# Performance work log

Hardware: AMD Instinct MI355X
Metric: run time of the kernel (lower is better)

The kernel has to match this reference:

```python
import jax, jax.numpy as jnp
import numpy as np

DIM, HEADS, DHEAD = 256, 8, 64
HID = HEADS * DHEAD


def _elu1(x):
    # F.elu(x) + 1 == exp(x) for x<0, x+1 for x>=0
    return jnp.where(x > 0, x + 1.0, jnp.exp(x))


def setup_inputs() -> dict:
    key = jax.random.key(0)
    ks = jax.random.split(key, 6)
    B, H, W = 8, 64, 64
    x = jax.random.normal(ks[0], (B, DIM, H, W), dtype=jnp.float32)
    contact_map = jax.random.uniform(ks[1], (B, 1, H, W), dtype=jnp.float32)
    s_qkv = 1.0 / np.sqrt(DIM)
    Wqkv = jax.random.normal(ks[2], (3 * HID, DIM), dtype=jnp.float32) * s_qkv
    s_out = 1.0 / np.sqrt(HID)
    Wout = jax.random.normal(ks[3], (DIM, HID), dtype=jnp.float32) * s_out
    bout = jax.random.normal(ks[4], (DIM,), dtype=jnp.float32) * 0.01
    contact_scale = jnp.float32(0.1)
    return {"x": x, "contact_map": contact_map, "Wqkv": Wqkv,
            "Wout": Wout, "bout": bout, "contact_scale": contact_scale}


def reference(x, contact_map, Wqkv, Wout, bout, contact_scale):
    b, c, h, w = x.shape
    n = h * w
    xf = x.reshape(b, c, n)                                  # b c n
    qkv = jnp.einsum('oc,bcn->bon', Wqkv, xf)                # b (3*H*D) n
    qkv = qkv.reshape(b, 3, HEADS, DHEAD, n)                 # qkv-major channel order
    q = _elu1(qkv[:, 0])                                     # b h d n
    k = _elu1(qkv[:, 1])
    v = qkv[:, 2]
    cm = contact_map.reshape(b, 1, 1, n)                     # b 1 1 n
    k = k * (1.0 + contact_scale * cm)
    kv = jnp.einsum('bhdn,bhen->bhde', k, v)                 # b h d e
    ksum = k.sum(axis=-1)                                    # b h d
    z = 1.0 / (jnp.einsum('bhdn,bhd->bhn', q, ksum) + 1e-6)  # b h n
    out = jnp.einsum('bhde,bhdn->bhne', kv, q) * z[..., None]  # b h n e
    out = out.transpose(0, 1, 3, 2).reshape(b, HID, n)       # b (h d) n
    y = jnp.einsum('oc,bcn->bon', Wout, out) + bout[None, :, None]
    return y.reshape(b, -1, h, w)
```

## Files before the change

kernel.cpp:

```cpp
#include <hip/hip_runtime.h>
#include <stdint.h>


#define NPIX 4096
#define HIDC 512
#define DIMC 256
#define BATCH 8

typedef __attribute__((ext_vector_type(8))) short bf16x8;
typedef __attribute__((ext_vector_type(4))) float f32x4;
typedef __attribute__((ext_vector_type(16))) float f32x16;

__device__ __forceinline__ float bf2f(unsigned short h) {
    unsigned int u = ((unsigned int)h) << 16; float f;
    __builtin_memcpy(&f, &u, 4); return f;
}
__device__ __forceinline__ unsigned short f2bf(float f) {
    unsigned int u; __builtin_memcpy(&u, &f, 4);
    u += 0x7fffu + ((u >> 16) & 1u);
    return (unsigned short)(u >> 16);
}
__device__ __forceinline__ float elu1(float x) {
    return x > 0.f ? x + 1.f : __expf(x);
}
__device__ __forceinline__ void gl16(const unsigned short* g, unsigned short* l) {
    __builtin_amdgcn_global_load_lds(
        (__attribute__((address_space(1))) const void*)g,
        (__attribute__((address_space(3))) void*)l, 16, 0, 0);
}

__global__ __launch_bounds__(256) void k_convW(
    const float* __restrict__ Wqkv, const float* __restrict__ Wout,
    unsigned short* __restrict__ Wb, unsigned short* __restrict__ Wob)
{
    int i4 = (blockIdx.x * 256 + threadIdx.x) * 4;
    const int NW1 = 1536 * 256;
    float4 v; unsigned short* dst;
    if (i4 < NW1) { v = *(const float4*)&Wqkv[i4]; dst = Wb + i4; }
    else { int j = i4 - NW1; v = *(const float4*)&Wout[j]; dst = Wob + j; }
    ushort4 o; o.x = f2bf(v.x); o.y = f2bf(v.y); o.z = f2bf(v.z); o.w = f2bf(v.w);
    *(ushort4*)dst = o;
}

__global__ __launch_bounds__(256) void k_tx(
    const float* __restrict__ x, unsigned short* __restrict__ xT)
{
    __shared__ float tile[32][33];
    const int n0 = blockIdx.x * 32, c0 = blockIdx.y * 32, b = blockIdx.z;
    const int t = threadIdx.x;
    const int r = t >> 3, c4 = (t & 7) * 4;
    float4 v = *(const float4*)&x[((size_t)b * DIMC + c0 + r) * NPIX + n0 + c4];
    tile[r][c4 + 0] = v.x; tile[r][c4 + 1] = v.y;
    tile[r][c4 + 2] = v.z; tile[r][c4 + 3] = v.w;
    __syncthreads();
    ushort4 o;
    unsigned short* op = (unsigned short*)&o;
#pragma unroll
    for (int i = 0; i < 4; i++) op[i] = f2bf(tile[c4 + i][r]);
    *(ushort4*)&xT[((size_t)b * NPIX + n0 + r) * DIMC + c0 + c4] = o;
}


#define COMPUTE_TILE(SWAP, A0, A1)                                             \
    {                                                                          \
        const unsigned short* Wl = &Ws[cur][0];                                \
        _Pragma("unroll")                                                      \
        for (int ks = 0; ks < 16; ks++) {                                      \
            bf16x8 wf = *(const bf16x8*)&Wl[(wn * 32 + l31) * DIMC +           \
                                (((ks * 2 + lhi) ^ (l31 & 7)) * 8)];           \
            if (SWAP) {                                                        \
                A0 = __builtin_amdgcn_mfma_f32_32x32x16_bf16(wf, af[0][ks], A0, 0, 0, 0); \
                A1 = __builtin_amdgcn_mfma_f32_32x32x16_bf16(wf, af[1][ks], A1, 0, 0, 0); \
            } else {                                                           \
                A0 = __builtin_amdgcn_mfma_f32_32x32x16_bf16(af[0][ks], wf, A0, 0, 0, 0); \
                A1 = __builtin_amdgcn_mfma_f32_32x32x16_bf16(af[1][ks], wf, A1, 0, 0, 0); \
            }                                                                  \
        }                                                                      \
    }

__global__ __launch_bounds__(256, 1) void k_fused(
    const unsigned short* __restrict__ xT,
    const unsigned short* __restrict__ Wb,
    const float* __restrict__ cmp,
    const float* __restrict__ csp,
    unsigned short* __restrict__ qT,
    float* __restrict__ kvp,
    float* __restrict__ ksump)
{
    const int b  = blockIdx.y;
    const int m0 = blockIdx.x * 128;
    const int t  = threadIdx.x;
    const int wave = t >> 6, lane = t & 63;
    const int wm = wave >> 1, wn = wave & 1;
    const int l31 = lane & 31, lhi = lane >> 5;

    __shared__ unsigned short Ws[2][64 * DIMC];
    __shared__ unsigned short kS[64 * 128];
    __shared__ unsigned short vS[64 * 128];

    const float cs = *csp;

    auto stageW = [&](int wr, int buf) {
#pragma unroll
        for (int i = 0; i < 8; i++) {
            const int rowl = wave * 16 + i * 2 + (lane >> 5);
            const int ck = (lane & 31) ^ (rowl & 7);
            gl16(&Wb[(size_t)(wr + rowl) * DIMC + ck * 8],
                 &Ws[buf][(wave * 16 + i * 2) * DIMC]);
        }
    };

    stageW(0, 0);

    bf16x8 af[2][16];
    {
        const unsigned short* Ab = xT + ((size_t)b * NPIX + m0 + wm * 64) * DIMC;
#pragma unroll
        for (int pt = 0; pt < 2; pt++)
#pragma unroll
            for (int ks = 0; ks < 16; ks++)
                af[pt][ks] = *(const bf16x8*)&Ab[(size_t)(pt * 32 + l31) * DIMC
                                                 + ks * 16 + lhi * 8];
    }

    const float gv0 = 1.f + cs * cmp[(size_t)b * NPIX + m0 + wm * 64 + l31];
    const float gv1 = 1.f + cs * cmp[(size_t)b * NPIX + m0 + wm * 64 + 32 + l31];

    __syncthreads();
    int cur = 0;

    for (int nt = 0; nt < 8; nt++) {
        stageW(nt < 7 ? (nt + 1) * 64 : 512, cur ^ 1);
        f32x16 acc0, acc1;
#pragma unroll
        for (int r = 0; r < 16; r++) { acc0[r] = 0.f; acc1[r] = 0.f; }
        COMPUTE_TILE(0, acc0, acc1)
        const int chq = nt * 64 + wn * 32 + l31;
        unsigned short* qg = qT + ((size_t)b * NPIX + m0 + wm * 64) * HIDC + chq;
#pragma unroll
        for (int r = 0; r < 16; r++) {
            const int rp = (r & 3) + 8 * (r >> 2) + 4 * lhi;
            qg[(size_t)rp * HIDC]        = f2bf(elu1(acc0[r]));
            qg[(size_t)(32 + rp) * HIDC] = f2bf(elu1(acc1[r]));
        }
        __syncthreads();
        cur ^= 1;
    }

    for (int h = 0; h < 8; h++) {
        stageW(1024 + h * 64, cur ^ 1);
        f32x16 acc0, acc1;
#pragma unroll
        for (int r = 0; r < 16; r++) { acc0[r] = 0.f; acc1[r] = 0.f; }
        COMPUTE_TILE(1, acc0, acc1)
#pragma unroll
        for (int r = 0; r < 16; r++) {
            const int ch = wn * 32 + (r & 3) + 8 * (r >> 2) + 4 * lhi;
            const int sw = (ch & 7) << 3;
            const int p0 = wm * 64 + l31;
            kS[ch * 128 + (p0 ^ sw)]        = f2bf(elu1(acc0[r]) * gv0);
            kS[ch * 128 + ((p0 + 32) ^ sw)] = f2bf(elu1(acc1[r]) * gv1);
        }
        __syncthreads();
        {
            const int ch = t & 63, cb = (t >> 6) * 4;
            float s = 0.f;
#pragma unroll
            for (int j = 0; j < 4; j++) {
                const bf16x8 kr = *(const bf16x8*)&kS[ch * 128 + (((cb + j) ^ (ch & 7)) * 8)];
#pragma unroll
                for (int u = 0; u < 8; u++) s += bf2f(((const unsigned short*)&kr)[u]);
            }
            atomicAdd(&ksump[(size_t)(b * 8 + h) * 64 + ch], s);
        }
        cur ^= 1;

        if (h < 7) stageW(512 + (h + 1) * 64, cur ^ 1);
#pragma unroll
        for (int r = 0; r < 16; r++) { acc0[r] = 0.f; acc1[r] = 0.f; }
        COMPUTE_TILE(1, acc0, acc1)
#pragma unroll
        for (int r = 0; r < 16; r++) {
            const int ch = wn * 32 + (r & 3) + 8 * (r >> 2) + 4 * lhi;
            const int sw = (ch & 7) << 3;
            const int p0 = wm * 64 + l31;
            vS[ch * 128 + (p0 ^ sw)]        = f2bf(acc0[r]);
            vS[ch * 128 + ((p0 + 32) ^ sw)] = f2bf(acc1[r]);
        }
        __syncthreads();

        f32x16 kvacc;
#pragma unroll
        for (int r = 0; r < 16; r++) kvacc[r] = 0.f;
#pragma unroll
        for (int pk = 0; pk < 8; pk++) {
            const int co = (((pk * 2 + lhi) ^ (l31 & 7)) * 8);
            const bf16x8 kf = *(const bf16x8*)&kS[(wm * 32 + l31) * 128 + co];
            const bf16x8 vf = *(const bf16x8*)&vS[(wn * 32 + l31) * 128 + co];
            kvacc = __builtin_amdgcn_mfma_f32_32x32x16_bf16(kf, vf, kvacc, 0, 0, 0);
        }
        __syncthreads();
        float* kvb = kvp + (size_t)(b * 8 + h) * 4096;
#pragma unroll
        for (int r = 0; r < 16; r++) {
            const int d = wm * 32 + (r & 3) + 8 * (r >> 2) + 4 * lhi;
            atomicAdd(&kvb[d * 64 + wn * 32 + l31], kvacc[r]);
        }
        cur ^= 1;
    }
}

#define LS3 72
__global__ __launch_bounds__(256) void k_out(
    const unsigned short* __restrict__ qT,
    const float* __restrict__ kv, const float* __restrict__ ksum,
    unsigned short* __restrict__ outT)
{
    const int bh = blockIdx.y, p0 = blockIdx.x * 128;
    const int b = bh >> 3, h = bh & 7;
    const int t = threadIdx.x, wave = t >> 6, lane = t & 63;
    const int l31 = lane & 31, lhi = lane >> 5;

    __shared__ unsigned short Aq[128 * LS3];
    __shared__ unsigned short Bv[96 * LS3];

    const unsigned short* qg = qT + ((size_t)b * NPIX + p0) * HIDC + h * 64;
#pragma unroll
    for (int i = 0; i < 4; i++) {
        int idx = t + i * 256;
        int row = idx >> 3, c8 = (idx & 7) * 8;
        *(uint4*)&Aq[row * LS3 + c8] = *(const uint4*)&qg[(size_t)row * HIDC + c8];
    }
    const float* kvg = kv + (size_t)bh * 4096;
#pragma unroll
    for (int i = 0; i < 16; i++) {
        int idx = t + i * 256;
        int d = idx >> 6, e = idx & 63;
        Bv[e * LS3 + d] = f2bf(kvg[idx]);
    }
    if (t < 64) {
        float ksv = ksum[bh * 64 + t];
        unsigned short hi = f2bf(ksv);
        Bv[64 * LS3 + t] = hi;
        Bv[65 * LS3 + t] = f2bf(ksv - bf2f(hi));
    }
    for (int i = t; i < 30 * 64; i += 256)
        Bv[(66 + (i >> 6)) * LS3 + (i & 63)] = 0;
    __syncthreads();

    f32x16 acc[3];
#pragma unroll
    for (int j = 0; j < 3; j++)
#pragma unroll
        for (int r = 0; r < 16; r++) acc[j][r] = 0.f;

#pragma unroll
    for (int ksub = 0; ksub < 4; ksub++) {
        const int koff = ksub * 16 + lhi * 8;
        bf16x8 af = *(const bf16x8*)&Aq[(wave * 32 + l31) * LS3 + koff];
#pragma unroll
        for (int nf = 0; nf < 3; nf++) {
            bf16x8 bfg = *(const bf16x8*)&Bv[(nf * 32 + l31) * LS3 + koff];
            acc[nf] = __builtin_amdgcn_mfma_f32_32x32x16_bf16(af, bfg, acc[nf], 0, 0, 0);
        }
    }

    unsigned short* og = outT + ((size_t)b * NPIX + p0 + wave * 32) * HIDC + h * 64;
#pragma unroll
    for (int r = 0; r < 16; r++) {
        float hi = __shfl(acc[2][r], lane & 32);
        float lo = __shfl(acc[2][r], (lane & 32) | 1);
        float z = 1.f / (hi + lo + 1e-6f);
        int prow = (r & 3) + 8 * (r >> 2) + 4 * lhi;
#pragma unroll
        for (int nf = 0; nf < 2; nf++)
            og[(size_t)prow * HIDC + nf * 32 + l31] = f2bf(acc[nf][r] * z);
    }
}

__global__ __launch_bounds__(256) void k_y(
    const unsigned short* __restrict__ outT,
    const unsigned short* __restrict__ Wob,
    const float* __restrict__ bout,
    float* __restrict__ y)
{
    const int b  = blockIdx.z;
    const int m0 = blockIdx.x * 128;
    const int n0 = blockIdx.y * 128;
    const int t = threadIdx.x;
    const int wave = t >> 6, lane = t & 63;
    const int wm = wave >> 1, wn = wave & 1;
    const int lrow = lane & 15, quad = lane >> 4;

    __shared__ unsigned short As[128 * 64];
    __shared__ unsigned short Bs[128 * 64];

    const unsigned short* Ag = outT + ((size_t)b * NPIX + m0) * HIDC;
    const unsigned short* Bg = Wob + (size_t)n0 * HIDC;

    f32x4 acc[4][4];
#pragma unroll
    for (int i = 0; i < 4; i++)
#pragma unroll
        for (int j = 0; j < 4; j++) acc[i][j] = (f32x4){0.f, 0.f, 0.f, 0.f};

    const int r8  = lane >> 3;
    const int jg8 = (((lane & 7) ^ r8) & 7) * 8;
    const int xswA = (lrow & 7);

    for (int k0 = 0; k0 < HIDC; k0 += 64) {
#pragma unroll
        for (int i = 0; i < 4; i++) {
            const int rowg = wave * 32 + i * 8;
            gl16(&Ag[(size_t)(rowg + r8) * HIDC + k0 + jg8], &As[rowg * 64]);
            gl16(&Bg[(size_t)(rowg + r8) * HIDC + k0 + jg8], &Bs[rowg * 64]);
        }
        __syncthreads();
#pragma unroll
        for (int ksb = 0; ksb < 2; ksb++) {
            bf16x8 af[4], bfr[4];
#pragma unroll
            for (int mt = 0; mt < 4; mt++) {
                const int row = wm * 64 + mt * 16 + lrow;
                af[mt] = *(const bf16x8*)&As[row * 64 + (((ksb * 4 + quad) ^ xswA)) * 8];
            }
#pragma unroll
            for (int nt = 0; nt < 4; nt++) {
                const int row = wn * 64 + nt * 16 + lrow;
                bfr[nt] = *(const bf16x8*)&Bs[row * 64 + (((ksb * 4 + quad) ^ xswA)) * 8];
            }
#pragma unroll
            for (int mt = 0; mt < 4; mt++)
#pragma unroll
                for (int nt = 0; nt < 4; nt++)
                    acc[mt][nt] = __builtin_amdgcn_mfma_f32_16x16x32_bf16(
                        af[mt], bfr[nt], acc[mt][nt], 0, 0, 0);
        }
        __syncthreads();
    }

#pragma unroll
    for (int mt = 0; mt < 4; mt++) {
        const int pixel0 = m0 + wm * 64 + mt * 16 + quad * 4;
#pragma unroll
        for (int nt = 0; nt < 4; nt++) {
            const int o = n0 + wn * 64 + nt * 16 + lrow;
            const float bias = bout[o];
            f32x4 a = acc[mt][nt];
            float4 st; st.x = a[0] + bias; st.y = a[1] + bias;
            st.z = a[2] + bias; st.w = a[3] + bias;
            *(float4*)&y[((size_t)b * DIMC + o) * NPIX + pixel0] = st;
        }
    }
}

extern "C" void kernel_launch(void* const* d_in, const int* in_sizes, int n_in,
                              void* d_out, int out_size, void* d_ws, size_t ws_size,
                              hipStream_t stream) {
    (void)in_sizes; (void)n_in; (void)out_size; (void)ws_size;
    const float* x    = (const float*)d_in[0];
    const float* cm   = (const float*)d_in[1];
    const float* Wqkv = (const float*)d_in[2];
    const float* Wout = (const float*)d_in[3];
    const float* bout = (const float*)d_in[4];
    const float* csp  = (const float*)d_in[5];
    float* y = (float*)d_out;

    const size_t qn = (size_t)BATCH * HIDC * NPIX;
    char* ws = (char*)d_ws;
    unsigned short* qT   = (unsigned short*)ws;                 ws += qn * 2;
    unsigned short* outT = (unsigned short*)ws;                 ws += qn * 2;
    unsigned short* xT   = outT;
    float* kvp   = (float*)ws;                                  ws += (size_t)64 * 64 * 64 * 4;
    float* ksump = (float*)ws;                                  ws += (size_t)64 * 64 * 4;
    unsigned short* Wb  = (unsigned short*)ws;                  ws += (size_t)1536 * 256 * 2;
    unsigned short* Wob = (unsigned short*)ws;

    hipMemsetAsync(kvp, 0, ((size_t)64 * 64 * 64 + 64 * 64) * sizeof(float), stream);
    k_convW<<<512, 256, 0, stream>>>(Wqkv, Wout, Wb, Wob);
    k_tx   <<<dim3(128, 8, 8), 256, 0, stream>>>(x, xT);
    k_fused<<<dim3(32, 8),     256, 0, stream>>>(xT, Wb, cm, csp, qT, kvp, ksump);
    k_out  <<<dim3(32, 64),    256, 0, stream>>>(qT, kvp, ksump, outT);
    k_y    <<<dim3(32, 2, 8),  256, 0, stream>>>(outT, Wob, bout, y);
}
```

Baseline: 198.7 us.

## Halve fused QKV pixel tile, split K staging, raise occupancy to two blocks

The fused QKV/kv kernel now processes 64 pixels per block instead of 128, launching twice as many blocks (512 vs 256) with launch bounds allowing two blocks per CU. Weight tiles are staged in K-halves of 128 columns, which halves shared memory and register footprint (one accumulator and 16 A fragments per wave). The kv MFMA for head h is deferred into the next iteration to overlap with weight staging. The cost is more kv/ksum atomics (twice as many blocks contribute), more barriers per tile, and twice as much total weight traffic from L2.

New measurement: 235.8 us. +18.6%, slower.

```diff
diff --git a/kernel.cpp b/kernel.cpp
--- a/kernel.cpp
+++ b/kernel.cpp
@@ -61,24 +61,18 @@
 }
 
 
-#define COMPUTE_TILE(SWAP, A0, A1)                                             \
-    {                                                                          \
-        const unsigned short* Wl = &Ws[cur][0];                                \
-        _Pragma("unroll")                                                      \
-        for (int ks = 0; ks < 16; ks++) {                                      \
-            bf16x8 wf = *(const bf16x8*)&Wl[(wn * 32 + l31) * DIMC +           \
-                                (((ks * 2 + lhi) ^ (l31 & 7)) * 8)];           \
-            if (SWAP) {                                                        \
-                A0 = __builtin_amdgcn_mfma_f32_32x32x16_bf16(wf, af[0][ks], A0, 0, 0, 0); \
-                A1 = __builtin_amdgcn_mfma_f32_32x32x16_bf16(wf, af[1][ks], A1, 0, 0, 0); \
-            } else {                                                           \
-                A0 = __builtin_amdgcn_mfma_f32_32x32x16_bf16(af[0][ks], wf, A0, 0, 0, 0); \
-                A1 = __builtin_amdgcn_mfma_f32_32x32x16_bf16(af[1][ks], wf, A1, 0, 0, 0); \
-            }                                                                  \
-        }                                                                      \
-    }
-
-__global__ __launch_bounds__(256, 1) void k_fused(
+#define CHALF(ACC, KH, BUF, SWAP)                                              \
+    _Pragma("unroll")                                                          \
+    for (int ks = 0; ks < 8; ks++) {                                           \
+        bf16x8 wf = *(const bf16x8*)&Ws[BUF][(wn * 32 + l31) * 128 +           \
+                            (((ks * 2 + lhi) ^ (l31 & 7)) * 8)];               \
+        if (SWAP)                                                              \
+            ACC = __builtin_amdgcn_mfma_f32_32x32x16_bf16(wf, af[(KH) * 8 + ks], ACC, 0, 0, 0); \
+        else                                                                   \
+            ACC = __builtin_amdgcn_mfma_f32_32x32x16_bf16(af[(KH) * 8 + ks], wf, ACC, 0, 0, 0); \
+    }
+
+__global__ __launch_bounds__(256, 2) void k_fused(
     const unsigned short* __restrict__ xT,
     const unsigned short* __restrict__ Wb,
     const float* __restrict__ cmp,
@@ -88,125 +82,141 @@
     float* __restrict__ ksump)
 {
     const int b  = blockIdx.y;
-    const int m0 = blockIdx.x * 128;
+    const int m0 = blockIdx.x * 64;
     const int t  = threadIdx.x;
     const int wave = t >> 6, lane = t & 63;
     const int wm = wave >> 1, wn = wave & 1;
     const int l31 = lane & 31, lhi = lane >> 5;
 
-    __shared__ unsigned short Ws[2][64 * DIMC];
-    __shared__ unsigned short kS[64 * 128];
-    __shared__ unsigned short vS[64 * 128];
+    __shared__ unsigned short Ws[2][64 * 128];
+    __shared__ unsigned short kS[64 * 64];
+    __shared__ unsigned short vS[64 * 64];
 
     const float cs = *csp;
 
-    auto stageW = [&](int wr, int buf) {
-#pragma unroll
-        for (int i = 0; i < 8; i++) {
-            const int rowl = wave * 16 + i * 2 + (lane >> 5);
-            const int ck = (lane & 31) ^ (rowl & 7);
-            gl16(&Wb[(size_t)(wr + rowl) * DIMC + ck * 8],
-                 &Ws[buf][(wave * 16 + i * 2) * DIMC]);
+    auto stageW = [&](int R, int kh, int buf) {
+#pragma unroll
+        for (int i = 0; i < 4; i++) {
+            const int rowbase = wave * 16 + i * 4;
+            const int row = rowbase + (lane >> 4);
+            gl16(&Wb[(size_t)(R + row) * DIMC + kh * 128 +
+                     (((lane & 15) ^ (row & 7)) * 8)],
+                 &Ws[buf][rowbase * 128]);
         }
     };
 
-    stageW(0, 0);
-
-    bf16x8 af[2][16];
+    stageW(0, 0, 0);
+
+    bf16x8 af[16];
     {
-        const unsigned short* Ab = xT + ((size_t)b * NPIX + m0 + wm * 64) * DIMC;
-#pragma unroll
-        for (int pt = 0; pt < 2; pt++)
-#pragma unroll
-            for (int ks = 0; ks < 16; ks++)
-                af[pt][ks] = *(const bf16x8*)&Ab[(size_t)(pt * 32 + l31) * DIMC
-                                                 + ks * 16 + lhi * 8];
-    }
-
-    const float gv0 = 1.f + cs * cmp[(size_t)b * NPIX + m0 + wm * 64 + l31];
-    const float gv1 = 1.f + cs * cmp[(size_t)b * NPIX + m0 + wm * 64 + 32 + l31];
-
-    __syncthreads();
-    int cur = 0;
+        const unsigned short* Ab = xT + ((size_t)b * NPIX + m0 + wm * 32 + l31) * DIMC;
+#pragma unroll
+        for (int ks = 0; ks < 16; ks++)
+            af[ks] = *(const bf16x8*)&Ab[ks * 16 + lhi * 8];
+    }
+    const float gv = 1.f + cs * cmp[(size_t)b * NPIX + m0 + wm * 32 + l31];
 
     for (int nt = 0; nt < 8; nt++) {
-        stageW(nt < 7 ? (nt + 1) * 64 : 512, cur ^ 1);
-        f32x16 acc0, acc1;
-#pragma unroll
-        for (int r = 0; r < 16; r++) { acc0[r] = 0.f; acc1[r] = 0.f; }
-        COMPUTE_TILE(0, acc0, acc1)
-        const int chq = nt * 64 + wn * 32 + l31;
-        unsigned short* qg = qT + ((size_t)b * NPIX + m0 + wm * 64) * HIDC + chq;
+        __syncthreads();
+        stageW(nt * 64, 1, 1);
+        f32x16 acc;
+#pragma unroll
+        for (int r = 0; r < 16; r++) acc[r] = 0.f;
+        CHALF(acc, 0, 0, 0)
+        __syncthreads();
+        stageW(nt < 7 ? (nt + 1) * 64 : 512, 0, 0);
+        CHALF(acc, 1, 1, 0)
+        unsigned short* qg = qT + ((size_t)b * NPIX + m0 + wm * 32) * HIDC
+                           + nt * 64 + wn * 32 + l31;
 #pragma unroll
         for (int r = 0; r < 16; r++) {
             const int rp = (r & 3) + 8 * (r >> 2) + 4 * lhi;
-            qg[(size_t)rp * HIDC]        = f2bf(elu1(acc0[r]));
-            qg[(size_t)(32 + rp) * HIDC] = f2bf(elu1(acc1[r]));
-        }
-        __syncthreads();
-        cur ^= 1;
+            qg[(size_t)rp * HIDC] = f2bf(elu1(acc[r]));
+        }
     }
 
     for (int h = 0; h < 8; h++) {
-        stageW(1024 + h * 64, cur ^ 1);
-        f32x16 acc0, acc1;
-#pragma unroll
-        for (int r = 0; r < 16; r++) { acc0[r] = 0.f; acc1[r] = 0.f; }
-        COMPUTE_TILE(1, acc0, acc1)
+        __syncthreads();
+        stageW(512 + h * 64, 1, 1);
+        if (h > 0) {
+            f32x16 kvacc;
+#pragma unroll
+            for (int r = 0; r < 16; r++) kvacc[r] = 0.f;
+#pragma unroll
+            for (int pk = 0; pk < 4; pk++) {
+                const int co = ((pk * 2 + lhi) ^ (l31 & 7)) * 8;
+                bf16x8 kf = *(const bf16x8*)&kS[(wm * 32 + l31) * 64 + co];
+                bf16x8 vf = *(const bf16x8*)&vS[(wn * 32 + l31) * 64 + co];
+                kvacc = __builtin_amdgcn_mfma_f32_32x32x16_bf16(kf, vf, kvacc, 0, 0, 0);
+            }
+            float* kvb = kvp + (size_t)(b * 8 + (h - 1)) * 4096;
+#pragma unroll
+            for (int r = 0; r < 16; r++) {
+                const int d = wm * 32 + (r & 3) + 8 * (r >> 2) + 4 * lhi;
+                atomicAdd(&kvb[d * 64 + wn * 32 + l31], kvacc[r]);
+            }
+        }
+        f32x16 acc;
+#pragma unroll
+        for (int r = 0; r < 16; r++) acc[r] = 0.f;
+        CHALF(acc, 0, 0, 1)
+        __syncthreads();
+        stageW(1024 + h * 64, 0, 0);
+        CHALF(acc, 1, 1, 1)
 #pragma unroll
         for (int r = 0; r < 16; r++) {
             const int ch = wn * 32 + (r & 3) + 8 * (r >> 2) + 4 * lhi;
-            const int sw = (ch & 7) << 3;
-            const int p0 = wm * 64 + l31;
-            kS[ch * 128 + (p0 ^ sw)]        = f2bf(elu1(acc0[r]) * gv0);
-            kS[ch * 128 + ((p0 + 32) ^ sw)] = f2bf(elu1(acc1[r]) * gv1);
-        }
-        __syncthreads();
+            const int pixl = wm * 32 + l31;
+            kS[ch * 64 + (pixl ^ ((ch & 7) << 3))] = f2bf(elu1(acc[r]) * gv);
+        }
+
+        __syncthreads();
+        stageW(1024 + h * 64, 1, 1);
         {
-            const int ch = t & 63, cb = (t >> 6) * 4;
+            const int ch = t & 63, part = t >> 6;
             float s = 0.f;
 #pragma unroll
-            for (int j = 0; j < 4; j++) {
-                const bf16x8 kr = *(const bf16x8*)&kS[ch * 128 + (((cb + j) ^ (ch & 7)) * 8)];
+            for (int j2 = 0; j2 < 2; j2++) {
+                const int j = part * 2 + j2;
+                const bf16x8 kr = *(const bf16x8*)&kS[ch * 64 + ((j ^ (ch & 7)) * 8)];
 #pragma unroll
                 for (int u = 0; u < 8; u++) s += bf2f(((const unsigned short*)&kr)[u]);
             }
             atomicAdd(&ksump[(size_t)(b * 8 + h) * 64 + ch], s);
         }
-        cur ^= 1;
-
-        if (h < 7) stageW(512 + (h + 1) * 64, cur ^ 1);
-#pragma unroll
-        for (int r = 0; r < 16; r++) { acc0[r] = 0.f; acc1[r] = 0.f; }
-        COMPUTE_TILE(1, acc0, acc1)
+        f32x16 acc2;
+#pragma unroll
+        for (int r = 0; r < 16; r++) acc2[r] = 0.f;
+        CHALF(acc2, 0, 0, 1)
+        __syncthreads();
+        if (h < 7) stageW(512 + (h + 1) * 64, 0, 0);
+        CHALF(acc2, 1, 1, 1)
 #pragma unroll
         for (int r = 0; r < 16; r++) {
             const int ch = wn * 32 + (r & 3) + 8 * (r >> 2) + 4 * lhi;
-            const int sw = (ch & 7) << 3;
-            const int p0 = wm * 64 + l31;
-            vS[ch * 128 + (p0 ^ sw)]        = f2bf(acc0[r]);
-            vS[ch * 128 + ((p0 + 32) ^ sw)] = f2bf(acc1[r]);
-        }
-        __syncthreads();
-
+            const int pixl = wm * 32 + l31;
+            vS[ch * 64 + (pixl ^ ((ch & 7) << 3))] = f2bf(acc2[r]);
+        }
+    }
+
+    __syncthreads();
+    {
         f32x16 kvacc;
 #pragma unroll
         for (int r = 0; r < 16; r++) kvacc[r] = 0.f;
 #pragma unroll
-        for (int pk = 0; pk < 8; pk++) {
-            const int co = (((pk * 2 + lhi) ^ (l31 & 7)) * 8);
-            const bf16x8 kf = *(const bf16x8*)&kS[(wm * 32 + l31) * 128 + co];
-            const bf16x8 vf = *(const bf16x8*)&vS[(wn * 32 + l31) * 128 + co];
+        for (int pk = 0; pk < 4; pk++) {
+            const int co = ((pk * 2 + lhi) ^ (l31 & 7)) * 8;
+            bf16x8 kf = *(const bf16x8*)&kS[(wm * 32 + l31) * 64 + co];
+            bf16x8 vf = *(const bf16x8*)&vS[(wn * 32 + l31) * 64 + co];
             kvacc = __builtin_amdgcn_mfma_f32_32x32x16_bf16(kf, vf, kvacc, 0, 0, 0);
         }
-        __syncthreads();
-        float* kvb = kvp + (size_t)(b * 8 + h) * 4096;
+        float* kvb = kvp + (size_t)(b * 8 + 7) * 4096;
 #pragma unroll
         for (int r = 0; r < 16; r++) {
             const int d = wm * 32 + (r & 3) + 8 * (r >> 2) + 4 * lhi;
             atomicAdd(&kvb[d * 64 + wn * 32 + l31], kvacc[r]);
         }
-        cur ^= 1;
     }
 }
 
@@ -379,7 +389,7 @@
     hipMemsetAsync(kvp, 0, ((size_t)64 * 64 * 64 + 64 * 64) * sizeof(float), stream);
     k_convW<<<512, 256, 0, stream>>>(Wqkv, Wout, Wb, Wob);
     k_tx   <<<dim3(128, 8, 8), 256, 0, stream>>>(x, xT);
-    k_fused<<<dim3(32, 8),     256, 0, stream>>>(xT, Wb, cm, csp, qT, kvp, ksump);
+    k_fused<<<dim3(64, 8),     256, 0, stream>>>(xT, Wb, cm, csp, qT, kvp, ksump);
     k_out  <<<dim3(32, 64),    256, 0, stream>>>(qT, kvp, ksump, outT);
     k_y    <<<dim3(32, 2, 8),  256, 0, stream>>>(outT, Wob, bout, y);
 }
```
